# Performance work log

Measured on AMD Instinct MI355X. Metric: run time of the kernel, lower is better.

## Reference

```python
import jax, jax.numpy as jnp
import numpy as np

NUM_SAMPLES = 50      # init kwarg num_samples
EPS = 1e-08           # init kwarg epsilon
PENALTY = 1e-4        # probability penalty weight in forward term
REV_SCALE = 0.1       # reverse-term scaling
CHUNK = 1000          # chunk size for online 1-NN min reduction


def _barycenters(vertices, faces):
    # vertices: [N,3], faces: [F,3] -> [F,3]
    return vertices[faces].mean(axis=1)


def _euclid_dist_matrix(p1, p2):
    # p1: [A,3], p2: [B,3] -> [A,B] Euclidean distances (torch.cdist p=2)
    d2 = (jnp.sum(p1 * p1, axis=-1, keepdims=True)
          - 2.0 * p1 @ p2.T
          + jnp.sum(p2 * p2, axis=-1)[None, :])
    return jnp.sqrt(jnp.maximum(d2, 0.0))


def setup_inputs() -> dict:
    key = jax.random.key(0)
    k0, k1, k2, k3, k4 = jax.random.split(key, 5)
    original_vertices = jax.random.normal(k0, (20000, 3), dtype=jnp.float32)
    original_faces = jax.random.randint(k1, (30000, 3), 0, 20000)
    simplified_vertices = jax.random.normal(k2, (4000, 3), dtype=jnp.float32)
    simplified_faces = jax.random.randint(k3, (5000, 3), 0, 4000)
    face_probabilities = jax.random.uniform(k4, (5000,), dtype=jnp.float32)
    return {
        "original_vertices": original_vertices,
        "original_faces": original_faces,
        "simplified_vertices": simplified_vertices,
        "simplified_faces": simplified_faces,
        "face_probabilities": face_probabilities,
    }


def reference(original_vertices, original_faces, simplified_vertices,
              simplified_faces, face_probabilities):
    n_sf = simplified_faces.shape[0]
    # pad/truncate face_probabilities to number of simplified faces (static shapes)
    fp = jnp.pad(face_probabilities,
                 (0, max(0, n_sf - face_probabilities.shape[0])))[:n_sf]

    # ---- forward term: barycenter cdist + row-min ----
    sb = _barycenters(simplified_vertices, simplified_faces)   # [Fs,3]
    ob = _barycenters(original_vertices, original_faces)       # [Fo,3]
    dist = _euclid_dist_matrix(sb, ob)                         # [Fs,Fo]
    min_d = dist.min(axis=1)                                   # [Fs]
    forward_term = jnp.sum(fp * min_d) + PENALTY * jnp.sum(1.0 - fp)

    # ---- reverse term: barycentric sampling + 1-NN to original vertices ----
    rk1, rk2 = jax.random.split(jax.random.key(42))
    sqrt_r1 = jnp.sqrt(jax.random.uniform(rk1, (n_sf, NUM_SAMPLES, 1)))
    r2 = jax.random.uniform(rk2, (n_sf, NUM_SAMPLES, 1))
    fv = simplified_vertices[simplified_faces]                 # [Fs,3,3]
    a = 1.0 - sqrt_r1
    b = sqrt_r1 * (1.0 - r2)
    c = sqrt_r1 * r2
    samples = (a * fv[:, None, 0] + b * fv[:, None, 1]
               + c * fv[:, None, 2]).reshape(-1, 3)            # [Fs*S,3]

    tv = original_vertices
    tv2 = jnp.sum(tv * tv, axis=-1)                            # [Nov]

    def chunk_min(pts):  # pts: [CHUNK,3] -> [CHUNK] min Euclid distance
        d2 = (jnp.sum(pts * pts, axis=-1, keepdims=True)
              - 2.0 * pts @ tv.T + tv2[None, :])
        return jnp.sqrt(jnp.maximum(d2.min(axis=1), 0.0))

    n_pts = samples.shape[0]
    dists = jax.lax.map(chunk_min,
                        samples.reshape(n_pts // CHUNK, CHUNK, 3)).reshape(-1)
    scaled = dists / (dists.max() + EPS) * REV_SCALE
    reverse_term = jnp.sum(jnp.repeat(fp, NUM_SAMPLES) * scaled)

    return forward_term + reverse_term
```

## Files before the change

### kernel.cpp

```cpp
#include <hip/hip_runtime.h>
#include <stdint.h>
#include <float.h>

#define NUM_SAMPLES 50
#define EPSF 1e-8f
#define PENALTY 1e-4f
#define REV_SCALE 0.1f

#define G1 48
#define G1LO -5.0f
#define G1HI 5.0f
#define NCELL1 (G1*G1*G1)
#define G2 48
#define G2LO -3.5f
#define G2HI 3.5f
#define NCELL2 (G2*G2*G2)

#define NTOTALL (NCELL1 + NCELL2)
#define SCAN_BLOCKS (NTOTALL / 1024)
static_assert(NTOTALL % 1024 == 0, "scan tiling");

#define GS 8
#define QBLOCKS 4096

#define ACC_FLOATS 4096

__device__ __forceinline__ uint32_t rotl32(uint32_t v, int d) {
  return (v << d) | (v >> (32 - d));
}

__device__ __forceinline__ void threefry2x32(uint32_t k0, uint32_t k1,
                                             uint32_t x0, uint32_t x1,
                                             uint32_t& o0, uint32_t& o1) {
  const uint32_t k2 = k0 ^ k1 ^ 0x1BD11BDAu;
  x0 += k0; x1 += k1;
#define TF_ROUND(r) { x0 += x1; x1 = rotl32(x1, (r)); x1 ^= x0; }
  TF_ROUND(13) TF_ROUND(15) TF_ROUND(26) TF_ROUND(6)
  x0 += k1; x1 += k2 + 1u;
  TF_ROUND(17) TF_ROUND(29) TF_ROUND(16) TF_ROUND(24)
  x0 += k2; x1 += k0 + 2u;
  TF_ROUND(13) TF_ROUND(15) TF_ROUND(26) TF_ROUND(6)
  x0 += k0; x1 += k1 + 3u;
  TF_ROUND(17) TF_ROUND(29) TF_ROUND(16) TF_ROUND(24)
  x0 += k1; x1 += k2 + 4u;
  TF_ROUND(13) TF_ROUND(15) TF_ROUND(26) TF_ROUND(6)
  x0 += k2; x1 += k0 + 5u;
#undef TF_ROUND
  o0 = x0; o1 = x1;
}

__device__ __forceinline__ float bits_to_uniform(uint32_t bits) {
  return __uint_as_float((bits >> 9) | 0x3f800000u) - 1.0f;
}

__device__ __forceinline__ float jax_uniform_at(uint32_t k0, uint32_t k1, uint32_t idx) {
  uint32_t o0, o1;
  threefry2x32(k0, k1, 0u, idx, o0, o1);
  return bits_to_uniform(o0 ^ o1);
}

__device__ __forceinline__ int cell_coord(float p, float lo, float invh, int G) {
  int i = (int)floorf((p - lo) * invh);
  return min(max(i, 0), G - 1);
}

__device__ __forceinline__ float4 gen_sample(int id, const float* __restrict__ sv,
                                             const int* __restrict__ sfc,
                                             const float* __restrict__ fp, int NFP) {
  int face = id / NUM_SAMPLES;
  uint32_t a0, a1, b0, b1;
  threefry2x32(0u, 42u, 0u, 0u, a0, a1);
  threefry2x32(0u, 42u, 0u, 1u, b0, b1);
  float r1 = jax_uniform_at(a0, a1, (uint32_t)id);
  float r2 = jax_uniform_at(b0, b1, (uint32_t)id);
  float sr1 = sqrtf(r1);
  float ca = 1.0f - sr1;
  float cb = sr1 * (1.0f - r2);
  float cc = sr1 * r2;
  int va = sfc[3*face], vb = sfc[3*face+1], vc = sfc[3*face+2];
  float px = ca*sv[3*va]   + cb*sv[3*vb]   + cc*sv[3*vc];
  float py = ca*sv[3*va+1] + cb*sv[3*vb+1] + cc*sv[3*vc+1];
  float pz = ca*sv[3*va+2] + cb*sv[3*vb+2] + cc*sv[3*vc+2];
  float w = (face < NFP) ? fp[face] : 0.0f;
  return make_float4(px, py, pz, w);
}

__global__ __launch_bounds__(256) void prep_kernel(
    const float* __restrict__ ov, const int* __restrict__ ofc,
    const float* __restrict__ sv, const int* __restrict__ sfc,
    float4* __restrict__ ob4, float4* __restrict__ sb4, float4* __restrict__ ov4,
    int* __restrict__ cnt, int NOF, int NSF, int NOV) {
  int i = blockIdx.x * blockDim.x + threadIdx.x;
  if (i >= NOF + NSF + NOV) return;
  if (i < NOF) {
    int a = ofc[3*i], b = ofc[3*i+1], c = ofc[3*i+2];
    float x = (ov[3*a]   + ov[3*b]   + ov[3*c])   / 3.0f;
    float y = (ov[3*a+1] + ov[3*b+1] + ov[3*c+1]) / 3.0f;
    float z = (ov[3*a+2] + ov[3*b+2] + ov[3*c+2]) / 3.0f;
    ob4[i] = make_float4(x, y, z, x*x + y*y + z*z);
    const float invh = (float)G2 / (G2HI - G2LO);
    int cx = cell_coord(x, G2LO, invh, G2);
    int cy = cell_coord(y, G2LO, invh, G2);
    int cz = cell_coord(z, G2LO, invh, G2);
    atomicAdd(&cnt[NCELL1 + (cz*G2 + cy)*G2 + cx], 1);
  } else if (i < NOF + NSF) {
    int j = i - NOF;
    int a = sfc[3*j], b = sfc[3*j+1], c = sfc[3*j+2];
    float x = (sv[3*a]   + sv[3*b]   + sv[3*c])   / 3.0f;
    float y = (sv[3*a+1] + sv[3*b+1] + sv[3*c+1]) / 3.0f;
    float z = (sv[3*a+2] + sv[3*b+2] + sv[3*c+2]) / 3.0f;
    sb4[j] = make_float4(x, y, z, x*x + y*y + z*z);
  } else {
    int j = i - NOF - NSF;
    float x = ov[3*j], y = ov[3*j+1], z = ov[3*j+2];
    ov4[j] = make_float4(x, y, z, x*x + y*y + z*z);
    const float invh = (float)G1 / (G1HI - G1LO);
    int cx = cell_coord(x, G1LO, invh, G1);
    int cy = cell_coord(y, G1LO, invh, G1);
    int cz = cell_coord(z, G1LO, invh, G1);
    atomicAdd(&cnt[(cz*G1 + cy)*G1 + cx], 1);
  }
}

__global__ __launch_bounds__(256) void scan_kernel(
    const int4* __restrict__ cnt4, unsigned long long* __restrict__ gsum,
    int* __restrict__ cs, int* __restrict__ cur) {
  __shared__ int lds[256];
  __shared__ int wsum[4];
  __shared__ int boffS;
  int t = threadIdx.x;
  int gid = blockIdx.x * 256 + t;
  int4 c = cnt4[gid];
  int s01 = c.x + c.y;
  int tsum = s01 + c.z + c.w;
  lds[t] = tsum;
  __syncthreads();
  for (int d = 1; d < 256; d <<= 1) {
    int u = (t >= d) ? lds[t - d] : 0;
    __syncthreads();
    lds[t] += u;
    __syncthreads();
  }
  int incl = lds[t];
  int agg  = lds[255];
  if (t == 0)
    atomicExch(&gsum[blockIdx.x], (1ULL << 63) | (unsigned long long)(unsigned)agg);
  int pre = 0;
  if (t < (int)blockIdx.x) {
    unsigned long long v;
    while (!((v = __hip_atomic_load(&gsum[t], __ATOMIC_RELAXED,
                                    __HIP_MEMORY_SCOPE_AGENT)) >> 63)) { }
    pre = (int)(v & 0xFFFFFFFFULL);
  }
  for (int o = 32; o > 0; o >>= 1) pre += __shfl_down(pre, o);
  if ((t & 63) == 0) wsum[t >> 6] = pre;
  __syncthreads();
  if (t == 0) boffS = wsum[0] + wsum[1] + wsum[2] + wsum[3];
  __syncthreads();
  int base = boffS + incl - tsum;
  int4 o4;
  o4.x = base;
  o4.y = base + c.x;
  o4.z = base + s01;
  o4.w = base + s01 + c.z;
  ((int4*)cs)[gid] = o4;
  ((int4*)cur)[gid] = o4;
  if (blockIdx.x == gridDim.x - 1 && t == 255) cs[NTOTALL] = boffS + incl;
}

__global__ __launch_bounds__(256) void scatter_kernel(
    const float4* __restrict__ ov4, const float4* __restrict__ ob4,
    int* __restrict__ cur, float4* __restrict__ sorted, int NOV, int NOF) {
  int i = blockIdx.x * blockDim.x + threadIdx.x;
  if (i >= NOV + NOF) return;
  float4 p; int c;
  if (i < NOV) {
    p = ov4[i];
    const float invh = (float)G1 / (G1HI - G1LO);
    int cx = cell_coord(p.x, G1LO, invh, G1);
    int cy = cell_coord(p.y, G1LO, invh, G1);
    int cz = cell_coord(p.z, G1LO, invh, G1);
    c = (cz*G1 + cy)*G1 + cx;
  } else {
    p = ob4[i - NOV];
    const float invh = (float)G2 / (G2HI - G2LO);
    int cx = cell_coord(p.x, G2LO, invh, G2);
    int cy = cell_coord(p.y, G2LO, invh, G2);
    int cz = cell_coord(p.z, G2LO, invh, G2);
    c = NCELL1 + (cz*G2 + cy)*G2 + cx;
  }
  int idx = atomicAdd(&cur[c], 1);
  sorted[idx] = p;
}

__device__ __forceinline__ float group_min(float v) {
  for (int o = GS / 2; o > 0; o >>= 1) v = fminf(v, __shfl_xor(v, o, GS));
  return v;
}

__device__ float nn_group(float px, float py, float pz, float q2,
                          const int* __restrict__ cs, const float4* __restrict__ pts,
                          int G, float lo, float h, int cellofs, int lane) {
  const float invh = 1.0f / h;
  int ix = cell_coord(px, lo, invh, G);
  int iy = cell_coord(py, lo, invh, G);
  int iz = cell_coord(pz, lo, invh, G);
  float wxm = fmaxf(px - (lo + (float)ix * h), 0.0f);
  float wxp = fmaxf((lo + (float)(ix + 1) * h) - px, 0.0f);
  float wym = fmaxf(py - (lo + (float)iy * h), 0.0f);
  float wyp = fmaxf((lo + (float)(iy + 1) * h) - py, 0.0f);
  float wzm = fmaxf(pz - (lo + (float)iz * h), 0.0f);
  float wzp = fmaxf((lo + (float)(iz + 1) * h) - pz, 0.0f);
  float wmin = fminf(fminf(fminf(wxm, wxp), fminf(wym, wyp)), fminf(wzm, wzp));

  float m2x = -2.0f*px, m2y = -2.0f*py, m2z = -2.0f*pz;
  float best = FLT_MAX;
  for (int r = 0; r < G; ++r) {
    float bmin = group_min(best);
    float bestd2 = bmin + q2;
    if (r >= 1) {
      float bd = (float)(r - 1) * h + wmin;
      if (bestd2 <= bd * bd) break;
    }
    int z0 = max(iz - r, 0), z1 = min(iz + r, G - 1);
    int y0 = max(iy - r, 0), y1 = min(iy + r, G - 1);
    int x0 = max(ix - r, 0), x1 = min(ix + r, G - 1);
    float dxm = (float)(r - 1) * h + wxm;
    float dxp = (float)(r - 1) * h + wxp;
    for (int zz = z0; zz <= z1; ++zz) {
      int oz = zz - iz;
      int adz = abs(oz);
      float dz = (oz > 0) ? (float)(oz - 1) * h + wzp
               : (oz < 0) ? (float)(-oz - 1) * h + wzm : 0.0f;
      float dz2 = dz * dz;
      if (dz2 >= bestd2) continue;
      for (int yy = y0; yy <= y1; ++yy) {
        int oy = yy - iy;
        int ady = abs(oy);
        float dy = (oy > 0) ? (float)(oy - 1) * h + wyp
                 : (oy < 0) ? (float)(-oy - 1) * h + wym : 0.0f;
        float rowd2 = dz2 + dy * dy;
        if (rowd2 >= bestd2) continue;
        int rowbase = cellofs + (zz*G + yy)*G;
        if (adz == r || ady == r) {
          int s = cs[rowbase + x0];
          int e = cs[rowbase + x1 + 1];
          for (int i = s + lane; i < e; i += GS) {
            float4 v = pts[i];
            best = fminf(best, fmaf(v.z, m2z, fmaf(v.y, m2y, fmaf(v.x, m2x, v.w))));
          }
        } else {
          if (ix - r >= 0 && rowd2 + dxm * dxm < bestd2) {
            int cc = rowbase + ix - r;
            int s = cs[cc], e = cs[cc + 1];
            for (int i = s + lane; i < e; i += GS) {
              float4 v = pts[i];
              best = fminf(best, fmaf(v.z, m2z, fmaf(v.y, m2y, fmaf(v.x, m2x, v.w))));
            }
          }
          if (r > 0 && ix + r <= G - 1 && rowd2 + dxp * dxp < bestd2) {
            int cc = rowbase + ix + r;
            int s = cs[cc], e = cs[cc + 1];
            for (int i = s + lane; i < e; i += GS) {
              float4 v = pts[i];
              best = fminf(best, fmaf(v.z, m2z, fmaf(v.y, m2y, fmaf(v.x, m2x, v.w))));
            }
          }
        }
      }
    }
  }
  return group_min(best);
}

__global__ __launch_bounds__(256) void query_kernel(
    const float* __restrict__ fp, const float4* __restrict__ sb4,
    const float* __restrict__ sv, const int* __restrict__ sfc,
    const int* __restrict__ cs, const float4* __restrict__ sorted,
    float* __restrict__ acc, float* __restrict__ out,
    int NSF, int NFP, int nsamp) {
  const float h1 = (G1HI - G1LO) / (float)G1;
  const float h2 = (G2HI - G2LO) / (float)G2;
  int lane = threadIdx.x & (GS - 1);
  int grpInBlk = threadIdx.x / GS;
  const int grpsPerBlk = 256 / GS;
  int totalGroups = NSF + nsamp;
  float facc = 0.0f, racc = 0.0f, rmaxv = 0.0f;
  for (int g = blockIdx.x * grpsPerBlk + grpInBlk; g < totalGroups;
       g += gridDim.x * grpsPerBlk) {
    if (g < NSF) {
      float4 s = sb4[g];
      float best = nn_group(s.x, s.y, s.z, s.w, cs, sorted, G2, G2LO, h2, NCELL1, lane);
      if (lane == 0) {
        float mind = sqrtf(fmaxf(best + s.w, 0.0f));
        float p = (g < NFP) ? fp[g] : 0.0f;
        facc += p * mind;
      }
    } else {
      int sid = g - NSF;
      float4 s = gen_sample(sid, sv, sfc, fp, NFP);
      float q2 = s.x*s.x + s.y*s.y + s.z*s.z;
      float best = nn_group(s.x, s.y, s.z, q2, cs, sorted, G1, G1LO, h1, 0, lane);
      if (lane == 0) {
        float d = sqrtf(fmaxf(best + q2, 0.0f));
        racc += s.w * d;
        rmaxv = fmaxf(rmaxv, d);
      }
    }
  }
  __shared__ float sF[4], sR[4], sM[4];
  __shared__ int isLast;
  __shared__ float stash[4];
  for (int o = 32; o > 0; o >>= 1) {
    facc += __shfl_down(facc, o);
    racc += __shfl_down(racc, o);
    rmaxv = fmaxf(rmaxv, __shfl_down(rmaxv, o));
  }
  int wid = threadIdx.x >> 6;
  if ((threadIdx.x & 63) == 0) { sF[wid] = facc; sR[wid] = racc; sM[wid] = rmaxv; }
  __syncthreads();
  if (threadIdx.x == 0) {
    float tf = sF[0] + sF[1] + sF[2] + sF[3];
    float tr = sR[0] + sR[1] + sR[2] + sR[3];
    float tm = fmaxf(fmaxf(sM[0], sM[1]), fmaxf(sM[2], sM[3]));
    int slot = (blockIdx.x & 63) * 16;
    atomicAdd(&acc[slot], tf);
    atomicAdd(&acc[1024 + slot], tr);
    atomicMax((int*)acc + 2048 + slot, __float_as_int(tm));
    __threadfence();
    int old = atomicAdd((int*)acc + 3072, 1);
    isLast = (old == (int)gridDim.x - 1) ? 1 : 0;
  }
  __syncthreads();
  if (!isLast) return;

  __shared__ float red[256];
  int t = threadIdx.x;
  float fsum = 0.0f, rsum = 0.0f, rmx = 0.0f;
  if (t < 64)        fsum = atomicAdd(&acc[t * 16], 0.0f);
  else if (t < 128)  rsum = atomicAdd(&acc[1024 + (t - 64) * 16], 0.0f);
  else if (t < 192)  rmx  = __int_as_float(atomicMax((int*)acc + 2048 + (t - 128) * 16, 0));
  float sfp = 0.0f;
  for (int i = t; i < NSF; i += 256) sfp += (i < NFP) ? fp[i] : 0.0f;

  red[t] = fsum; __syncthreads();
  for (int o = 128; o > 0; o >>= 1) { if (t < o) red[t] += red[t + o]; __syncthreads(); }
  if (t == 0) stash[0] = red[0];
  __syncthreads();
  red[t] = rsum; __syncthreads();
  for (int o = 128; o > 0; o >>= 1) { if (t < o) red[t] += red[t + o]; __syncthreads(); }
  if (t == 0) stash[1] = red[0];
  __syncthreads();
  red[t] = rmx; __syncthreads();
  for (int o = 128; o > 0; o >>= 1) { if (t < o) red[t] = fmaxf(red[t], red[t + o]); __syncthreads(); }
  if (t == 0) stash[2] = red[0];
  __syncthreads();
  red[t] = sfp; __syncthreads();
  for (int o = 128; o > 0; o >>= 1) { if (t < o) red[t] += red[t + o]; __syncthreads(); }
  if (t == 0) {
    float fwd = stash[0] + PENALTY * ((float)NSF - red[0]);
    float rev = stash[1] * (REV_SCALE / (stash[2] + EPSF));
    out[0] = fwd + rev;
  }
}

extern "C" void kernel_launch(void* const* d_in, const int* in_sizes, int n_in,
                              void* d_out, int out_size, void* d_ws, size_t ws_size,
                              hipStream_t stream) {
  const float* ov  = (const float*)d_in[0];
  const int*   ofc = (const int*)  d_in[1];
  const float* sv  = (const float*)d_in[2];
  const int*   sfc = (const int*)  d_in[3];
  const float* fp  = (const float*)d_in[4];
  float* out = (float*)d_out;

  int NOV = in_sizes[0] / 3;
  int NOF = in_sizes[1] / 3;
  int NSF = in_sizes[3] / 3;
  int NFP = in_sizes[4];
  int nsamp = NSF * NUM_SAMPLES;

  char* w = (char*)d_ws;
  float* acc = (float*)w;                       w += ACC_FLOATS * 4;
  unsigned long long* gsum = (unsigned long long*)w; w += 2048;
  int*   cnt = (int*)w;                         w += (size_t)NTOTALL * 4;
  size_t zeroBytes = (size_t)(w - (char*)d_ws);
  int*   cs  = (int*)w;                         w += (size_t)(NTOTALL + 16) * 4;
  int*   cur = (int*)w;                         w += (size_t)NTOTALL * 4;
  float4* ob4    = (float4*)w;  w += (size_t)NOF * 16;
  float4* sb4    = (float4*)w;  w += (size_t)NSF * 16;
  float4* ov4    = (float4*)w;  w += (size_t)NOV * 16;
  float4* sorted = (float4*)w;  w += (size_t)(NOV + NOF) * 16;

  hipMemsetAsync(d_ws, 0, zeroBytes, stream);

  int total = NOF + NSF + NOV;
  hipLaunchKernelGGL(prep_kernel, dim3((total + 255) / 256), dim3(256), 0, stream,
                     ov, ofc, sv, sfc, ob4, sb4, ov4, cnt, NOF, NSF, NOV);

  hipLaunchKernelGGL(scan_kernel, dim3(SCAN_BLOCKS), dim3(256), 0, stream,
                     (const int4*)cnt, gsum, cs, cur);

  hipLaunchKernelGGL(scatter_kernel, dim3((NOV + NOF + 255) / 256), dim3(256), 0, stream,
                     ov4, ob4, cur, sorted, NOV, NOF);

  hipLaunchKernelGGL(query_kernel, dim3(QBLOCKS), dim3(256), 0, stream,
                     fp, sb4, sv, sfc, cs, sorted, acc, out, NSF, NFP, nsamp);
}
```

Baseline: 227.8 us.

## Fuse prep, scan and scatter into one persistent kernel with grid barriers

Merges the three grid-build kernels into a single persistent launch of 216 blocks that uses atomic grid barriers between phases, and zeroes the cell counters inside the kernel instead of through the memset. This removes two kernel launches and their gaps and shrinks the memset. In exchange it relies on all 216 blocks being co-resident for the spin barriers, and grid-stride loops over fewer threads lower parallelism in the prep and scatter phases.

Measured after the change: 344.3 us. 1.51x slower.

```diff
diff --git a/kernel.cpp b/kernel.cpp
--- a/kernel.cpp
+++ b/kernel.cpp
@@ -17,8 +17,8 @@
 #define NCELL2 (G2*G2*G2)
 
 #define NTOTALL (NCELL1 + NCELL2)
-#define SCAN_BLOCKS (NTOTALL / 1024)
-static_assert(NTOTALL % 1024 == 0, "scan tiling");
+#define BGRID 216
+static_assert(NTOTALL == BGRID * 1024, "scan tiling");
 
 #define GS 8
 #define QBLOCKS 4096
@@ -85,112 +85,134 @@
   return make_float4(px, py, pz, w);
 }
 
-__global__ __launch_bounds__(256) void prep_kernel(
+__device__ __forceinline__ void grid_barrier(int* ctr, int target) {
+  __syncthreads();
+  __threadfence();
+  if (threadIdx.x == 0) {
+    __hip_atomic_fetch_add(ctr, 1, __ATOMIC_RELEASE, __HIP_MEMORY_SCOPE_AGENT);
+    while (__hip_atomic_load(ctr, __ATOMIC_ACQUIRE, __HIP_MEMORY_SCOPE_AGENT) < target) {}
+  }
+  __syncthreads();
+  __threadfence();
+}
+
+__global__ __launch_bounds__(256) void build_kernel(
     const float* __restrict__ ov, const int* __restrict__ ofc,
     const float* __restrict__ sv, const int* __restrict__ sfc,
     float4* __restrict__ ob4, float4* __restrict__ sb4, float4* __restrict__ ov4,
-    int* __restrict__ cnt, int NOF, int NSF, int NOV) {
-  int i = blockIdx.x * blockDim.x + threadIdx.x;
-  if (i >= NOF + NSF + NOV) return;
-  if (i < NOF) {
-    int a = ofc[3*i], b = ofc[3*i+1], c = ofc[3*i+2];
-    float x = (ov[3*a]   + ov[3*b]   + ov[3*c])   / 3.0f;
-    float y = (ov[3*a+1] + ov[3*b+1] + ov[3*c+1]) / 3.0f;
-    float z = (ov[3*a+2] + ov[3*b+2] + ov[3*c+2]) / 3.0f;
-    ob4[i] = make_float4(x, y, z, x*x + y*y + z*z);
-    const float invh = (float)G2 / (G2HI - G2LO);
-    int cx = cell_coord(x, G2LO, invh, G2);
-    int cy = cell_coord(y, G2LO, invh, G2);
-    int cz = cell_coord(z, G2LO, invh, G2);
-    atomicAdd(&cnt[NCELL1 + (cz*G2 + cy)*G2 + cx], 1);
-  } else if (i < NOF + NSF) {
-    int j = i - NOF;
-    int a = sfc[3*j], b = sfc[3*j+1], c = sfc[3*j+2];
-    float x = (sv[3*a]   + sv[3*b]   + sv[3*c])   / 3.0f;
-    float y = (sv[3*a+1] + sv[3*b+1] + sv[3*c+1]) / 3.0f;
-    float z = (sv[3*a+2] + sv[3*b+2] + sv[3*c+2]) / 3.0f;
-    sb4[j] = make_float4(x, y, z, x*x + y*y + z*z);
-  } else {
-    int j = i - NOF - NSF;
-    float x = ov[3*j], y = ov[3*j+1], z = ov[3*j+2];
-    ov4[j] = make_float4(x, y, z, x*x + y*y + z*z);
-    const float invh = (float)G1 / (G1HI - G1LO);
-    int cx = cell_coord(x, G1LO, invh, G1);
-    int cy = cell_coord(y, G1LO, invh, G1);
-    int cz = cell_coord(z, G1LO, invh, G1);
-    atomicAdd(&cnt[(cz*G1 + cy)*G1 + cx], 1);
-  }
-}
-
-__global__ __launch_bounds__(256) void scan_kernel(
-    const int4* __restrict__ cnt4, unsigned long long* __restrict__ gsum,
-    int* __restrict__ cs, int* __restrict__ cur) {
-  __shared__ int lds[256];
-  __shared__ int wsum[4];
-  __shared__ int boffS;
-  int t = threadIdx.x;
-  int gid = blockIdx.x * 256 + t;
-  int4 c = cnt4[gid];
-  int s01 = c.x + c.y;
-  int tsum = s01 + c.z + c.w;
-  lds[t] = tsum;
-  __syncthreads();
-  for (int d = 1; d < 256; d <<= 1) {
-    int u = (t >= d) ? lds[t - d] : 0;
+    int* __restrict__ cnt, unsigned long long* __restrict__ gsum,
+    int* __restrict__ bar, int* __restrict__ cs, int* __restrict__ cur,
+    float4* __restrict__ sorted, int NOF, int NSF, int NOV) {
+  const int t = threadIdx.x;
+  const int bid = (int)blockIdx.x;
+  const int gtid = bid * 256 + t;
+  const int nth = BGRID * 256;
+
+  ((int4*)cnt)[gtid] = make_int4(0, 0, 0, 0);
+  grid_barrier(&bar[0], BGRID);
+
+  {
+    int total = NOF + NSF + NOV;
+    for (int i = gtid; i < total; i += nth) {
+      if (i < NOF) {
+        int a = ofc[3*i], b = ofc[3*i+1], c = ofc[3*i+2];
+        float x = (ov[3*a]   + ov[3*b]   + ov[3*c])   / 3.0f;
+        float y = (ov[3*a+1] + ov[3*b+1] + ov[3*c+1]) / 3.0f;
+        float z = (ov[3*a+2] + ov[3*b+2] + ov[3*c+2]) / 3.0f;
+        ob4[i] = make_float4(x, y, z, x*x + y*y + z*z);
+        const float invh = (float)G2 / (G2HI - G2LO);
+        int cx = cell_coord(x, G2LO, invh, G2);
+        int cy = cell_coord(y, G2LO, invh, G2);
+        int cz = cell_coord(z, G2LO, invh, G2);
+        atomicAdd(&cnt[NCELL1 + (cz*G2 + cy)*G2 + cx], 1);
+      } else if (i < NOF + NSF) {
+        int j = i - NOF;
+        int a = sfc[3*j], b = sfc[3*j+1], c = sfc[3*j+2];
+        float x = (sv[3*a]   + sv[3*b]   + sv[3*c])   / 3.0f;
+        float y = (sv[3*a+1] + sv[3*b+1] + sv[3*c+1]) / 3.0f;
+        float z = (sv[3*a+2] + sv[3*b+2] + sv[3*c+2]) / 3.0f;
+        sb4[j] = make_float4(x, y, z, x*x + y*y + z*z);
+      } else {
+        int j = i - NOF - NSF;
+        float x = ov[3*j], y = ov[3*j+1], z = ov[3*j+2];
+        ov4[j] = make_float4(x, y, z, x*x + y*y + z*z);
+        const float invh = (float)G1 / (G1HI - G1LO);
+        int cx = cell_coord(x, G1LO, invh, G1);
+        int cy = cell_coord(y, G1LO, invh, G1);
+        int cz = cell_coord(z, G1LO, invh, G1);
+        atomicAdd(&cnt[(cz*G1 + cy)*G1 + cx], 1);
+      }
+    }
+  }
+  grid_barrier(&bar[1], BGRID);
+
+  {
+    __shared__ int lds[256];
+    __shared__ int wsum[4];
+    __shared__ int boffS;
+    int gid = bid * 256 + t;
+    int4 c = ((const int4*)cnt)[gid];
+    int s01 = c.x + c.y;
+    int tsum = s01 + c.z + c.w;
+    lds[t] = tsum;
     __syncthreads();
-    lds[t] += u;
+    for (int d = 1; d < 256; d <<= 1) {
+      int u = (t >= d) ? lds[t - d] : 0;
+      __syncthreads();
+      lds[t] += u;
+      __syncthreads();
+    }
+    int incl = lds[t];
+    int agg  = lds[255];
+    if (t == 0)
+      atomicExch(&gsum[bid], (1ULL << 63) | (unsigned long long)(unsigned)agg);
+    int pre = 0;
+    if (t < bid) {
+      unsigned long long v;
+      while (!((v = __hip_atomic_load(&gsum[t], __ATOMIC_RELAXED,
+                                      __HIP_MEMORY_SCOPE_AGENT)) >> 63)) { }
+      pre = (int)(v & 0xFFFFFFFFULL);
+    }
+    for (int o = 32; o > 0; o >>= 1) pre += __shfl_down(pre, o);
+    if ((t & 63) == 0) wsum[t >> 6] = pre;
     __syncthreads();
-  }
-  int incl = lds[t];
-  int agg  = lds[255];
-  if (t == 0)
-    atomicExch(&gsum[blockIdx.x], (1ULL << 63) | (unsigned long long)(unsigned)agg);
-  int pre = 0;
-  if (t < (int)blockIdx.x) {
-    unsigned long long v;
-    while (!((v = __hip_atomic_load(&gsum[t], __ATOMIC_RELAXED,
-                                    __HIP_MEMORY_SCOPE_AGENT)) >> 63)) { }
-    pre = (int)(v & 0xFFFFFFFFULL);
-  }
-  for (int o = 32; o > 0; o >>= 1) pre += __shfl_down(pre, o);
-  if ((t & 63) == 0) wsum[t >> 6] = pre;
-  __syncthreads();
-  if (t == 0) boffS = wsum[0] + wsum[1] + wsum[2] + wsum[3];
-  __syncthreads();
-  int base = boffS + incl - tsum;
-  int4 o4;
-  o4.x = base;
-  o4.y = base + c.x;
-  o4.z = base + s01;
-  o4.w = base + s01 + c.z;
-  ((int4*)cs)[gid] = o4;
-  ((int4*)cur)[gid] = o4;
-  if (blockIdx.x == gridDim.x - 1 && t == 255) cs[NTOTALL] = boffS + incl;
-}
-
-__global__ __launch_bounds__(256) void scatter_kernel(
-    const float4* __restrict__ ov4, const float4* __restrict__ ob4,
-    int* __restrict__ cur, float4* __restrict__ sorted, int NOV, int NOF) {
-  int i = blockIdx.x * blockDim.x + threadIdx.x;
-  if (i >= NOV + NOF) return;
-  float4 p; int c;
-  if (i < NOV) {
-    p = ov4[i];
-    const float invh = (float)G1 / (G1HI - G1LO);
-    int cx = cell_coord(p.x, G1LO, invh, G1);
-    int cy = cell_coord(p.y, G1LO, invh, G1);
-    int cz = cell_coord(p.z, G1LO, invh, G1);
-    c = (cz*G1 + cy)*G1 + cx;
-  } else {
-    p = ob4[i - NOV];
-    const float invh = (float)G2 / (G2HI - G2LO);
-    int cx = cell_coord(p.x, G2LO, invh, G2);
-    int cy = cell_coord(p.y, G2LO, invh, G2);
-    int cz = cell_coord(p.z, G2LO, invh, G2);
-    c = NCELL1 + (cz*G2 + cy)*G2 + cx;
-  }
-  int idx = atomicAdd(&cur[c], 1);
-  sorted[idx] = p;
+    if (t == 0) boffS = wsum[0] + wsum[1] + wsum[2] + wsum[3];
+    __syncthreads();
+    int base = boffS + incl - tsum;
+    int4 o4;
+    o4.x = base;
+    o4.y = base + c.x;
+    o4.z = base + s01;
+    o4.w = base + s01 + c.z;
+    ((int4*)cs)[gid] = o4;
+    ((int4*)cur)[gid] = o4;
+    if (bid == BGRID - 1 && t == 255) cs[NTOTALL] = boffS + incl;
+  }
+  grid_barrier(&bar[2], BGRID);
+
+  {
+    int stotal = NOV + NOF;
+    for (int i = gtid; i < stotal; i += nth) {
+      float4 p; int c;
+      if (i < NOV) {
+        p = ov4[i];
+        const float invh = (float)G1 / (G1HI - G1LO);
+        int cx = cell_coord(p.x, G1LO, invh, G1);
+        int cy = cell_coord(p.y, G1LO, invh, G1);
+        int cz = cell_coord(p.z, G1LO, invh, G1);
+        c = (cz*G1 + cy)*G1 + cx;
+      } else {
+        p = ob4[i - NOV];
+        const float invh = (float)G2 / (G2HI - G2LO);
+        int cx = cell_coord(p.x, G2LO, invh, G2);
+        int cy = cell_coord(p.y, G2LO, invh, G2);
+        int cz = cell_coord(p.z, G2LO, invh, G2);
+        c = NCELL1 + (cz*G2 + cy)*G2 + cx;
+      }
+      int idx = atomicAdd(&cur[c], 1);
+      sorted[idx] = p;
+    }
+  }
 }
 
 __device__ __forceinline__ float group_min(float v) {
@@ -383,8 +405,9 @@
   char* w = (char*)d_ws;
   float* acc = (float*)w;                       w += ACC_FLOATS * 4;
   unsigned long long* gsum = (unsigned long long*)w; w += 2048;
+  int*   bar = (int*)w;                         w += 64;
+  size_t zeroBytes = (size_t)(w - (char*)d_ws);
   int*   cnt = (int*)w;                         w += (size_t)NTOTALL * 4;
-  size_t zeroBytes = (size_t)(w - (char*)d_ws);
   int*   cs  = (int*)w;                         w += (size_t)(NTOTALL + 16) * 4;
   int*   cur = (int*)w;                         w += (size_t)NTOTALL * 4;
   float4* ob4    = (float4*)w;  w += (size_t)NOF * 16;
@@ -394,15 +417,9 @@
 
   hipMemsetAsync(d_ws, 0, zeroBytes, stream);
 
-  int total = NOF + NSF + NOV;
-  hipLaunchKernelGGL(prep_kernel, dim3((total + 255) / 256), dim3(256), 0, stream,
-                     ov, ofc, sv, sfc, ob4, sb4, ov4, cnt, NOF, NSF, NOV);
-
-  hipLaunchKernelGGL(scan_kernel, dim3(SCAN_BLOCKS), dim3(256), 0, stream,
-                     (const int4*)cnt, gsum, cs, cur);
-
-  hipLaunchKernelGGL(scatter_kernel, dim3((NOV + NOF + 255) / 256), dim3(256), 0, stream,
-                     ov4, ob4, cur, sorted, NOV, NOF);
+  hipLaunchKernelGGL(build_kernel, dim3(BGRID), dim3(256), 0, stream,
+                     ov, ofc, sv, sfc, ob4, sb4, ov4,
+                     cnt, gsum, bar, cs, cur, sorted, NOF, NSF, NOV);
 
   hipLaunchKernelGGL(query_kernel, dim3(QBLOCKS), dim3(256), 0, stream,
                      fp, sb4, sv, sfc, cs, sorted, acc, out, NSF, NFP, nsamp);
```
